# Kernel tuning notes

Measured on AMD Instinct MI355X. Metric: run time of the kernel, lower is better.

## Reference

```python
import jax, jax.numpy as jnp
import numpy as np

B, T, D = 8, 2048, 256
EPS_NORM = 1e-8
EPS_LN = 1e-6


def _layer_norm(x, gamma, beta):
    mu = jnp.mean(x, axis=-1, keepdims=True)
    var = jnp.var(x, axis=-1, keepdims=True)
    return (x - mu) * jax.lax.rsqrt(var + EPS_LN) * gamma + beta


def setup_inputs() -> dict:
    key = jax.random.key(0)
    ks = jax.random.split(key, 8)
    xav = np.sqrt(2.0 / (D + D)).astype(np.float32)  # xavier_uniform-ish scale
    a_fea = jax.random.normal(ks[0], (B, T, D), jnp.float32)
    v_fea = jax.random.normal(ks[1], (B, T, D), jnp.float32)
    Wv1 = jax.random.normal(ks[2], (D, D), jnp.float32) * xav
    Wv2 = jax.random.normal(ks[3], (D, D), jnp.float32) * xav
    Wa1 = jax.random.normal(ks[4], (D, D), jnp.float32) * xav
    Wa2 = jax.random.normal(ks[5], (D, D), jnp.float32) * xav
    ln_gamma = jnp.ones((D,), jnp.float32)
    ln_beta = jnp.zeros((D,), jnp.float32)
    thr_val = jnp.asarray(0.099, jnp.float32)
    return {"a_fea": a_fea, "v_fea": v_fea, "Wv1": Wv1, "Wv2": Wv2,
            "Wa1": Wa1, "Wa2": Wa2, "ln_gamma": ln_gamma, "ln_beta": ln_beta,
            "thr_val": thr_val}


def reference(a_fea, v_fea, Wv1, Wv2, Wa1, Wa2, ln_gamma, ln_beta, thr_val):
    # Dropout is identity in eval mode. Linear(bias=False): x @ W^T; here W is [in, out].
    v_b1 = jax.nn.relu(jnp.einsum('btd,dh->bth', v_fea, Wv1))
    v_b2 = jax.nn.relu(jnp.einsum('btd,dh->bth', v_fea, Wv2))
    a_b1 = jax.nn.relu(jnp.einsum('btd,dh->bth', a_fea, Wa1))
    a_b2 = jax.nn.relu(jnp.einsum('btd,dh->bth', a_fea, Wa2))

    scale = 1.0 / jnp.sqrt(jnp.asarray(v_b2.shape[2], jnp.float32))
    # relu-gated cross-modal scores [B, Tv, Ta]
    beta = jax.nn.relu(jnp.einsum('bvh,bah->bva', v_b2, a_b1) * scale)

    # v->a: normalize over audio axis, threshold-sparsify
    beta_va = beta / (jnp.sum(beta, axis=-1, keepdims=True) + EPS_NORM)
    gamma_va = jnp.where(beta_va > thr_val, beta_va, 0.0)
    # a->v: transpose of UN-normalized beta (faithful to source ordering)
    beta_av = jnp.swapaxes(beta, 1, 2)
    beta_av = beta_av / (jnp.sum(beta_av, axis=-1, keepdims=True) + EPS_NORM)
    gamma_av = jnp.where(beta_av > thr_val, beta_av, 0.0)

    a_pos = jnp.einsum('bva,bah->bvh', gamma_va, a_b2)
    v_pos = jnp.einsum('bav,bvh->bah', gamma_av, v_b1)

    v_psp = _layer_norm(v_fea + a_pos, ln_gamma, ln_beta)
    a_psp = _layer_norm(a_fea + v_pos, ln_gamma, ln_beta)
    return (v_psp + a_psp) * 0.5
```

## Files before the change

### kernel.cpp

```cpp
#include <hip/hip_runtime.h>
#include <stdint.h>

#define B_ 8
#define T_ 2048
#define D_ 256
#define M_ (B_*T_)

typedef uint16_t u16;
typedef __attribute__((ext_vector_type(8))) short   short8;
typedef __attribute__((ext_vector_type(8))) __bf16  bf16x8;
typedef __attribute__((ext_vector_type(4))) float   f32x4;
typedef __attribute__((ext_vector_type(4))) uint32_t u32x4;

__device__ __forceinline__ float bf2f(u16 b){
    union { uint32_t u; float f; } v; v.u = ((uint32_t)b) << 16; return v.f;
}
__device__ __forceinline__ u16 f2bf(float f){
    union { float f; uint32_t u; } v; v.f = f;
    uint32_t u = v.u;
    u += 0x7FFFu + ((u >> 16) & 1u);
    return (u16)(u >> 16);
}

typedef __attribute__((address_space(1))) void gvoid;
typedef __attribute__((address_space(3))) void lvoid;
__device__ __forceinline__ void gl16(const void* g, void* l){
    __builtin_amdgcn_global_load_lds((gvoid*)(unsigned long long)g, (lvoid*)l, 16, 0, 0);
}

__global__ void k_detect(const uint32_t* g, int* flag){
    *flag = (g[0] == 0x3F803F80u) ? 0 : 1;
}

struct WtArgs { const void* w[4]; u16* wt[4]; const int* flag; };

__global__ __launch_bounds__(256) void k_wt(WtArgs a){
    int f32in = *a.flag;
    int m = blockIdx.y;
    int d = blockIdx.x;
    int h = threadIdx.x;
    float val;
    if (f32in) val = ((const float*)a.w[m])[(size_t)d * D_ + h];
    else       val = bf2f(((const u16*)a.w[m])[(size_t)d * D_ + h]);
    a.wt[m][(size_t)h * D_ + d] = f2bf(val);
}

struct ProjArgs { const void* x[4]; const u16* wt[4]; u16* y[4]; u16* yt[4]; const int* flag; };

__global__ __launch_bounds__(256) void k_proj(ProjArgs args){
    __shared__ __align__(16) u16 Xs[128][72];
    __shared__ __align__(16) u16 Ws[128][72];
    int f32in = *args.flag;
    int id = blockIdx.x;
    int m  = id & 127;
    int vh = id >> 7;
    int hh = vh & 1;
    int v  = vh >> 1;
    const u16* Wt = args.wt[v];
    u16*       Y  = args.y[v];
    u16*       YT = args.yt[v];
    int t_base = m * 128;
    int h_base = hh * 128;

    int tid  = threadIdx.x;
    int w    = tid >> 6, lane = tid & 63;
    int wm   = w >> 1, wn = w & 1;
    int l15  = lane & 15, quad = lane >> 4;

    int srow = tid >> 1;
    int shalf = tid & 1;

    f32x4 acc[4][4];
#pragma unroll
    for (int i = 0; i < 4; ++i)
#pragma unroll
        for (int j = 0; j < 4; ++j) acc[i][j] = (f32x4){0.f,0.f,0.f,0.f};

    float4 pXf[8];
    short8 pXb[4];
    short8 pW[4];

    const float* Xf = (const float*)args.x[v] + (size_t)(t_base + srow)*D_ + shalf*32;
    const u16*   Xb = (const u16*)args.x[v]   + (size_t)(t_base + srow)*D_ + shalf*32;
    const u16*   Wp = Wt + (size_t)(h_base + srow)*D_ + shalf*32;

    if (f32in){
#pragma unroll
        for (int i = 0; i < 8; ++i) pXf[i] = *(const float4*)(Xf + i*4);
    } else {
#pragma unroll
        for (int i = 0; i < 4; ++i) pXb[i] = *(const short8*)(Xb + i*8);
    }
#pragma unroll
    for (int i = 0; i < 4; ++i) pW[i] = *(const short8*)(Wp + i*8);

    for (int k0 = 0; k0 < D_; k0 += 64){
        __syncthreads();
        if (f32in){
#pragma unroll
            for (int i = 0; i < 4; ++i){
                float4 a0 = pXf[i*2], a1 = pXf[i*2+1];
                short8 o;
                o[0]=(short)f2bf(a0.x); o[1]=(short)f2bf(a0.y); o[2]=(short)f2bf(a0.z); o[3]=(short)f2bf(a0.w);
                o[4]=(short)f2bf(a1.x); o[5]=(short)f2bf(a1.y); o[6]=(short)f2bf(a1.z); o[7]=(short)f2bf(a1.w);
                *(short8*)(&Xs[srow][shalf*32 + i*8]) = o;
            }
        } else {
#pragma unroll
            for (int i = 0; i < 4; ++i) *(short8*)(&Xs[srow][shalf*32 + i*8]) = pXb[i];
        }
#pragma unroll
        for (int i = 0; i < 4; ++i) *(short8*)(&Ws[srow][shalf*32 + i*8]) = pW[i];

        int kn = k0 + 64;
        if (kn < D_){
            if (f32in){
#pragma unroll
                for (int i = 0; i < 8; ++i) pXf[i] = *(const float4*)(Xf + kn + i*4);
            } else {
#pragma unroll
                for (int i = 0; i < 4; ++i) pXb[i] = *(const short8*)(Xb + kn + i*8);
            }
#pragma unroll
            for (int i = 0; i < 4; ++i) pW[i] = *(const short8*)(Wp + kn + i*8);
        }
        __syncthreads();

#pragma unroll
        for (int kc = 0; kc < 2; ++kc){
            bf16x8 af[4], bf[4];
#pragma unroll
            for (int i = 0; i < 4; ++i){
                af[i] = __builtin_bit_cast(bf16x8,
                         *(const short8*)(&Xs[wm*64 + i*16 + l15][kc*32 + quad*8]));
                bf[i] = __builtin_bit_cast(bf16x8,
                         *(const short8*)(&Ws[wn*64 + i*16 + l15][kc*32 + quad*8]));
            }
#pragma unroll
            for (int mt = 0; mt < 4; ++mt)
#pragma unroll
                for (int nt = 0; nt < 4; ++nt)
                    acc[mt][nt] = __builtin_amdgcn_mfma_f32_16x16x32_bf16(
                                      af[mt], bf[nt], acc[mt][nt], 0, 0, 0);
        }
    }

    int v0 = t_base + wm*64;
    int h0 = h_base + wn*64;
#pragma unroll
    for (int mt = 0; mt < 4; ++mt){
#pragma unroll
        for (int nt = 0; nt < 4; ++nt){
            int col = h0 + nt*16 + l15;
            u16 q[4];
#pragma unroll
            for (int r = 0; r < 4; ++r){
                float s = acc[mt][nt][r]; s = s > 0.f ? s : 0.f;
                q[r] = f2bf(s);
            }
            if (Y){
#pragma unroll
                for (int r = 0; r < 4; ++r)
                    Y[(size_t)(v0 + mt*16 + quad*4 + r)*D_ + col] = q[r];
            }
            if (YT){
                int row0 = v0 + mt*16 + quad*4;
                int bb   = row0 >> 11;
                int tl   = row0 & (T_-1);
                uint2 pk;
                pk.x = (uint32_t)q[0] | ((uint32_t)q[1] << 16);
                pk.y = (uint32_t)q[2] | ((uint32_t)q[3] << 16);
                *(uint2*)(YT + ((size_t)(bb*D_ + col))*T_ + tl) = pk;
            }
        }
    }
}

__global__ __launch_bounds__(256) void k_score(const u16* vb2, const u16* ab1,
                                               u16* beta, u16* betaT,
                                               float* rowsum, float* colsum){
    __shared__ __align__(16) u16 As[128][72];
    __shared__ __align__(16) u16 Bs[128][72];
    int id = blockIdx.x;
    int b  = id & 7;
    int t  = id >> 3;
    int mb = t & 15;
    int ab = t >> 4;
    int tid  = threadIdx.x;
    int w    = tid >> 6, lane = tid & 63;
    int wm   = w >> 1, wn = w & 1;
    int l15  = lane & 15, quad = lane >> 4;
    int v_base = mb*128;
    int a_base = ab*128;

    const u16* vb = vb2 + (size_t)b*T_*D_;
    const u16* an = ab1 + (size_t)b*T_*D_;
    u16*   bbp = beta  + (size_t)b*T_*T_;
    u16*   bbt = betaT + (size_t)b*T_*T_;
    float* rs  = rowsum + b*T_;
    float* cs  = colsum + b*T_;

    int kk = tid & 7;
    int mm = tid >> 3;

    f32x4 acc[4][4];
#pragma unroll
    for (int i = 0; i < 4; ++i)
#pragma unroll
        for (int j = 0; j < 4; ++j) acc[i][j] = (f32x4){0.f,0.f,0.f,0.f};

    short8 pA[4], pB[4];
#pragma unroll
    for (int i = 0; i < 4; ++i){
        int row = mm + i*32;
        pA[i] = *(const short8*)(vb + (size_t)(v_base + row)*D_ + kk*8);
        pB[i] = *(const short8*)(an + (size_t)(a_base + row)*D_ + kk*8);
    }

    for (int k0 = 0; k0 < D_; k0 += 64){
        __syncthreads();
#pragma unroll
        for (int i = 0; i < 4; ++i){
            int row = mm + i*32;
            *(short8*)(&As[row][kk*8]) = pA[i];
            *(short8*)(&Bs[row][kk*8]) = pB[i];
        }
        int kn = k0 + 64;
        if (kn < D_){
#pragma unroll
            for (int i = 0; i < 4; ++i){
                int row = mm + i*32;
                pA[i] = *(const short8*)(vb + (size_t)(v_base + row)*D_ + kn + kk*8);
                pB[i] = *(const short8*)(an + (size_t)(a_base + row)*D_ + kn + kk*8);
            }
        }
        __syncthreads();

#pragma unroll
        for (int kc = 0; kc < 2; ++kc){
            bf16x8 af[4], bf[4];
#pragma unroll
            for (int i = 0; i < 4; ++i){
                af[i] = __builtin_bit_cast(bf16x8,
                         *(const short8*)(&As[wm*64 + i*16 + l15][kc*32 + quad*8]));
                bf[i] = __builtin_bit_cast(bf16x8,
                         *(const short8*)(&Bs[wn*64 + i*16 + l15][kc*32 + quad*8]));
            }
#pragma unroll
            for (int mt = 0; mt < 4; ++mt)
#pragma unroll
                for (int nt = 0; nt < 4; ++nt)
                    acc[mt][nt] = __builtin_amdgcn_mfma_f32_16x16x32_bf16(
                                      af[mt], bf[nt], acc[mt][nt], 0, 0, 0);
        }
    }

    int v0 = v_base + wm*64;
    int a0 = a_base + wn*64;
    float rsum[4][4];
    float csum[4] = {0.f,0.f,0.f,0.f};
#pragma unroll
    for (int mt = 0; mt < 4; ++mt)
#pragma unroll
        for (int r = 0; r < 4; ++r) rsum[mt][r] = 0.f;

#pragma unroll
    for (int mt = 0; mt < 4; ++mt){
#pragma unroll
        for (int nt = 0; nt < 4; ++nt){
            u16 q[4];
#pragma unroll
            for (int r = 0; r < 4; ++r){
                float s = acc[mt][nt][r] * 0.0625f;
                s = s > 0.f ? s : 0.f;
                q[r] = f2bf(s);
                bbp[(size_t)(v0 + mt*16 + quad*4 + r)*T_ + a0 + nt*16 + l15] = q[r];
                rsum[mt][r] += s;
                csum[nt]    += s;
            }
            uint2 pk;
            pk.x = (uint32_t)q[0] | ((uint32_t)q[1] << 16);
            pk.y = (uint32_t)q[2] | ((uint32_t)q[3] << 16);
            *(uint2*)(bbt + (size_t)(a0 + nt*16 + l15)*T_ + v0 + mt*16 + quad*4) = pk;
        }
    }
#pragma unroll
    for (int mt = 0; mt < 4; ++mt){
#pragma unroll
        for (int r = 0; r < 4; ++r){
            float v = rsum[mt][r];
            v += __shfl_xor(v, 1);
            v += __shfl_xor(v, 2);
            v += __shfl_xor(v, 4);
            v += __shfl_xor(v, 8);
            if (l15 == 0) atomicAdd(&rs[v0 + mt*16 + quad*4 + r], v);
        }
    }
#pragma unroll
    for (int nt = 0; nt < 4; ++nt){
        float v = csum[nt];
        v += __shfl_xor(v, 16);
        v += __shfl_xor(v, 32);
        if (quad == 0) atomicAdd(&cs[a0 + nt*16 + l15], v);
    }
}

__global__ __launch_bounds__(256) void k_pos4(const u16* beta, const u16* betaT,
                                              const u16* ab2T, const u16* vb1T,
                                              const float* rowsum, const float* colsum,
                                              const void* thrp, const int* flag,
                                              u16* apos, u16* vpos){
    __shared__ __align__(16) u16 SL[2][2][128*64];
    int f32in = *flag;
    int id = blockIdx.x;
    int nb    = id & 1;
    int mb    = (id >> 1) & 15;
    int b     = (id >> 5) & 7;
    int which = id >> 8;

    const u16* A   = (which ? betaT : beta) + (size_t)b*T_*T_;
    const u16* Bt  = (which ? vb1T  : ab2T) + (size_t)b*T_*D_;
    const float* nrm = (which ? colsum : rowsum) + b*T_;
    u16* outb = (which ? vpos : apos) + (size_t)b*T_*D_;

    float thr = f32in ? *(const float*)thrp : bf2f(*(const u16*)thrp);

    int tid = threadIdx.x;
    int w = tid >> 6, lane = tid & 63;
    int l15 = lane & 15, quad = lane >> 4;

    int m0 = mb * 128;
    int h0 = nb * 128;

    int srow = w*32 + (lane >> 3);
    int schk = (lane & 7) ^ ((lane >> 3) & 7);
    const u16* gA = A  + (size_t)(m0 + srow)*T_ + schk*8;
    const u16* gB = Bt + (size_t)(h0 + srow)*T_ + schk*8;

    uint32_t thp[2];
#pragma unroll
    for (int i = 0; i < 2; ++i){
        float ts = thr * (nrm[m0 + w*32 + i*16 + l15] + 1e-8f);
        union { float f; uint32_t u; } cv; cv.f = ts;
        uint32_t th16 = cv.u >> 16;
        thp[i] = th16 * 0x10001u;
    }

    f32x4 acc[2][8];
#pragma unroll
    for (int i = 0; i < 2; ++i)
#pragma unroll
        for (int j = 0; j < 8; ++j) acc[i][j] = (f32x4){0.f,0.f,0.f,0.f};

#pragma unroll
    for (int c = 0; c < 4; ++c){
        gl16(gA + (size_t)c*8*T_, &SL[0][0][(w*32 + c*8)*64]);
        gl16(gB + (size_t)c*8*T_, &SL[0][1][(w*32 + c*8)*64]);
    }

    int q = 0;
    for (int k0 = 0; k0 < T_; k0 += 64){
        __syncthreads();
        int kn = k0 + 64;
        if (kn < T_){
#pragma unroll
            for (int c = 0; c < 4; ++c){
                gl16(gA + (size_t)c*8*T_ + kn, &SL[q^1][0][(w*32 + c*8)*64]);
                gl16(gB + (size_t)c*8*T_ + kn, &SL[q^1][1][(w*32 + c*8)*64]);
            }
        }
        const u16* Asb = &SL[q][0][0];
        const u16* Bsb = &SL[q][1][0];
#pragma unroll
        for (int kc = 0; kc < 2; ++kc){
            int sw = ((kc*4 + quad) ^ (l15 & 7)) * 8;
            bf16x8 af[2];
#pragma unroll
            for (int i = 0; i < 2; ++i){
                u32x4 ra = *(const u32x4*)(Asb + (size_t)(w*32 + i*16 + l15)*64 + sw);
                u32x4 om;
#pragma unroll
                for (int jd = 0; jd < 4; ++jd){
                    uint32_t t, m;
                    asm("v_pk_sub_u16 %0, %1, %2" : "=v"(t) : "v"(thp[i]), "v"(ra[jd]));
                    asm("v_pk_ashrrev_i16 %0, 15, %1" : "=v"(m) : "v"(t));
                    om[jd] = ra[jd] & m;
                }
                af[i] = __builtin_bit_cast(bf16x8, om);
            }
#pragma unroll
            for (int nt = 0; nt < 8; ++nt){
                bf16x8 bfr = __builtin_bit_cast(bf16x8,
                              *(const short8*)(Bsb + (size_t)(nt*16 + l15)*64 + sw));
                acc[0][nt] = __builtin_amdgcn_mfma_f32_16x16x32_bf16(
                                  af[0], bfr, acc[0][nt], 0, 0, 0);
                acc[1][nt] = __builtin_amdgcn_mfma_f32_16x16x32_bf16(
                                  af[1], bfr, acc[1][nt], 0, 0, 0);
            }
        }
        q ^= 1;
    }

#pragma unroll
    for (int i = 0; i < 2; ++i){
#pragma unroll
        for (int r = 0; r < 4; ++r){
            int row = m0 + w*32 + i*16 + quad*4 + r;
            float iv = 1.f / (nrm[row] + 1e-8f);
#pragma unroll
            for (int nt = 0; nt < 8; ++nt)
                outb[(size_t)row*D_ + h0 + nt*16 + l15] =
                    f2bf(acc[i][nt][r] * iv);
        }
    }
}

__global__ __launch_bounds__(256) void k_ln(const void* vfea, const void* afea,
                                            const u16* apos, const u16* vpos,
                                            const void* g, const void* lnb,
                                            const int* flag, void* out){
    int f32in = *flag;
    int row = blockIdx.x;
    int c   = threadIdx.x;
    size_t idx = (size_t)row * D_ + c;
    float xv = f32in ? ((const float*)vfea)[idx] : bf2f(((const u16*)vfea)[idx]);
    float xa = f32in ? ((const float*)afea)[idx] : bf2f(((const u16*)afea)[idx]);
    float x1 = xv + bf2f(apos[idx]);
    float x2 = xa + bf2f(vpos[idx]);
    float s1 = x1, q1 = x1*x1, s2 = x2, q2 = x2*x2;
#pragma unroll
    for (int off = 1; off < 64; off <<= 1){
        s1 += __shfl_xor(s1, off);
        q1 += __shfl_xor(q1, off);
        s2 += __shfl_xor(s2, off);
        q2 += __shfl_xor(q2, off);
    }
    __shared__ float red[4][4];
    int wave = threadIdx.x >> 6;
    if ((threadIdx.x & 63) == 0){
        red[0][wave] = s1; red[1][wave] = q1; red[2][wave] = s2; red[3][wave] = q2;
    }
    __syncthreads();
    s1 = red[0][0]+red[0][1]+red[0][2]+red[0][3];
    q1 = red[1][0]+red[1][1]+red[1][2]+red[1][3];
    s2 = red[2][0]+red[2][1]+red[2][2]+red[2][3];
    q2 = red[3][0]+red[3][1]+red[3][2]+red[3][3];
    const float invD = 1.f / (float)D_;
    float mu1 = s1*invD, mu2 = s2*invD;
    float var1 = q1*invD - mu1*mu1;
    float var2 = q2*invD - mu2*mu2;
    float rs1 = rsqrtf(var1 + 1e-6f);
    float rs2 = rsqrtf(var2 + 1e-6f);
    float gg = f32in ? ((const float*)g)[c]   : bf2f(((const u16*)g)[c]);
    float bv = f32in ? ((const float*)lnb)[c] : bf2f(((const u16*)lnb)[c]);
    float y = 0.5f * (((x1-mu1)*rs1)*gg + bv + ((x2-mu2)*rs2)*gg + bv);
    if (f32in) ((float*)out)[idx] = y;
    else       ((u16*)out)[idx]   = f2bf(y);
}

extern "C" void kernel_launch(void* const* d_in, const int* in_sizes, int n_in,
                              void* d_out, int out_size, void* d_ws, size_t ws_size,
                              hipStream_t stream){
    (void)in_sizes; (void)n_in; (void)out_size; (void)ws_size;
    const void* a_fea = d_in[0];
    const void* v_fea = d_in[1];
    const void* Wv1   = d_in[2];
    const void* Wv2   = d_in[3];
    const void* Wa1   = d_in[4];
    const void* Wa2   = d_in[5];
    const void* lng   = d_in[6];
    const void* lnb   = d_in[7];
    const void* thrp  = d_in[8];
    char* ws = (char*)d_ws;

    const size_t ACT  = (size_t)M_ * D_ * 2;
    const size_t BETA = (size_t)B_ * T_ * T_ * 2;
    size_t off_wt    = 0;
    size_t off_vb2   = 524288;
    size_t off_ab1   = off_vb2  + ACT;
    size_t off_vb1T  = off_ab1  + ACT;
    size_t off_ab2T  = off_vb1T + ACT;
    size_t off_beta  = off_ab2T + ACT;
    size_t off_betaT = off_beta  + BETA;
    size_t off_rsum  = off_betaT + BETA;
    size_t off_csum  = off_rsum + (size_t)B_*T_*4;
    size_t off_apos  = off_csum + (size_t)B_*T_*4;
    size_t off_vpos  = off_apos + ACT;
    size_t off_flag  = off_vpos + ACT;

    u16* wt0   = (u16*)(ws + off_wt);
    u16* vb2   = (u16*)(ws + off_vb2);
    u16* ab1   = (u16*)(ws + off_ab1);
    u16* vb1T  = (u16*)(ws + off_vb1T);
    u16* ab2T  = (u16*)(ws + off_ab2T);
    u16* beta  = (u16*)(ws + off_beta);
    u16* betaT = (u16*)(ws + off_betaT);
    float* rowsum = (float*)(ws + off_rsum);
    float* colsum = (float*)(ws + off_csum);
    u16*   apos   = (u16*)(ws + off_apos);
    u16*   vpos   = (u16*)(ws + off_vpos);
    int*   flag   = (int*)(ws + off_flag);

    hipMemsetAsync(ws + off_rsum, 0, 2 * (size_t)B_ * T_ * sizeof(float), stream);

    k_detect<<<1, 1, 0, stream>>>((const uint32_t*)lng, flag);

    WtArgs wa;
    wa.w[0] = Wv1; wa.w[1] = Wv2; wa.w[2] = Wa1; wa.w[3] = Wa2;
    for (int i = 0; i < 4; ++i) wa.wt[i] = wt0 + (size_t)i * D_ * D_;
    wa.flag = flag;
    k_wt<<<dim3(256,4), 256, 0, stream>>>(wa);

    ProjArgs pa;
    pa.x[0] = v_fea; pa.x[1] = v_fea; pa.x[2] = a_fea; pa.x[3] = a_fea;
    for (int i = 0; i < 4; ++i) pa.wt[i] = wa.wt[i];
    pa.y[0] = nullptr; pa.y[1] = vb2; pa.y[2] = ab1; pa.y[3] = nullptr;
    pa.yt[0] = vb1T;   pa.yt[1] = nullptr; pa.yt[2] = nullptr; pa.yt[3] = ab2T;
    pa.flag = flag;
    k_proj<<<4*2*(M_/128), 256, 0, stream>>>(pa);

    k_score<<<8*16*16, 256, 0, stream>>>(vb2, ab1, beta, betaT, rowsum, colsum);

    k_pos4<<<512, 256, 0, stream>>>(beta, betaT, ab2T, vb1T, rowsum, colsum,
                                    thrp, flag, apos, vpos);

    k_ln<<<M_, 256, 0, stream>>>(v_fea, a_fea, apos, vpos, lng, lnb, flag, d_out);
}
```

Baseline: 247.9 us.

## Store beta once in tiled layout and read its transpose via ds_read_b64_tr_b16

The score kernel no longer writes a separate transposed copy of the beta matrix. It writes beta once, in 128x128 tiles. The aggregation kernel loads those tiles directly for the v->a side and uses the LDS transpose-read instruction to get transposed fragments for the a->v side. This removes one 64MB write and the scattered transposed stores, at the cost of a more complex LDS load path with an explicit waitcnt. Block indices are also remapped so that blocks from the same batch are interleaved across XCDs.

```diff
diff --git a/kernel.cpp b/kernel.cpp
--- a/kernel.cpp
+++ b/kernel.cpp
@@ -24,6 +24,7 @@
 
 typedef __attribute__((address_space(1))) void gvoid;
 typedef __attribute__((address_space(3))) void lvoid;
+typedef __attribute__((address_space(3))) const u16 lds_cu16;
 __device__ __forceinline__ void gl16(const void* g, void* l){
     __builtin_amdgcn_global_load_lds((gvoid*)(unsigned long long)g, (lvoid*)l, 16, 0, 0);
 }
@@ -177,7 +178,7 @@
 }
 
 __global__ __launch_bounds__(256) void k_score(const u16* vb2, const u16* ab1,
-                                               u16* beta, u16* betaT,
+                                               u16* beta_t,
                                                float* rowsum, float* colsum){
     __shared__ __align__(16) u16 As[128][72];
     __shared__ __align__(16) u16 Bs[128][72];
@@ -195,8 +196,7 @@
 
     const u16* vb = vb2 + (size_t)b*T_*D_;
     const u16* an = ab1 + (size_t)b*T_*D_;
-    u16*   bbp = beta  + (size_t)b*T_*T_;
-    u16*   bbt = betaT + (size_t)b*T_*T_;
+    u16* tb = beta_t + (((size_t)b*16 + mb)*16 + ab)*16384;
     float* rs  = rowsum + b*T_;
     float* cs  = colsum + b*T_;
 
@@ -255,8 +255,6 @@
         }
     }
 
-    int v0 = v_base + wm*64;
-    int a0 = a_base + wn*64;
     float rsum[4][4];
     float csum[4] = {0.f,0.f,0.f,0.f};
 #pragma unroll
@@ -268,22 +266,19 @@
     for (int mt = 0; mt < 4; ++mt){
 #pragma unroll
         for (int nt = 0; nt < 4; ++nt){
-            u16 q[4];
+            int aa = wn*64 + nt*16 + l15;
 #pragma unroll
             for (int r = 0; r < 4; ++r){
                 float s = acc[mt][nt][r] * 0.0625f;
                 s = s > 0.f ? s : 0.f;
-                q[r] = f2bf(s);
-                bbp[(size_t)(v0 + mt*16 + quad*4 + r)*T_ + a0 + nt*16 + l15] = q[r];
+                tb[(size_t)(wm*64 + mt*16 + quad*4 + r)*128 + aa] = f2bf(s);
                 rsum[mt][r] += s;
                 csum[nt]    += s;
             }
-            uint2 pk;
-            pk.x = (uint32_t)q[0] | ((uint32_t)q[1] << 16);
-            pk.y = (uint32_t)q[2] | ((uint32_t)q[3] << 16);
-            *(uint2*)(bbt + (size_t)(a0 + nt*16 + l15)*T_ + v0 + mt*16 + quad*4) = pk;
-        }
-    }
+        }
+    }
+    int v0 = v_base + wm*64;
+    int a0 = a_base + wn*64;
 #pragma unroll
     for (int mt = 0; mt < 4; ++mt){
 #pragma unroll
@@ -305,20 +300,21 @@
     }
 }
 
-__global__ __launch_bounds__(256) void k_pos4(const u16* beta, const u16* betaT,
+__global__ __launch_bounds__(256) void k_pos6(const u16* beta_t,
                                               const u16* ab2T, const u16* vb1T,
                                               const float* rowsum, const float* colsum,
                                               const void* thrp, const int* flag,
                                               u16* apos, u16* vpos){
     __shared__ __align__(16) u16 SL[2][2][128*64];
     int f32in = *flag;
-    int id = blockIdx.x;
+    int s  = blockIdx.x;
+    int id = (s & 7) * 64 + (s >> 3);
     int nb    = id & 1;
     int mb    = (id >> 1) & 15;
     int b     = (id >> 5) & 7;
     int which = id >> 8;
 
-    const u16* A   = (which ? betaT : beta) + (size_t)b*T_*T_;
+    const u16* TB  = beta_t + (size_t)b*16*16*16384;
     const u16* Bt  = (which ? vb1T  : ab2T) + (size_t)b*T_*D_;
     const float* nrm = (which ? colsum : rowsum) + b*T_;
     u16* outb = (which ? vpos : apos) + (size_t)b*T_*D_;
@@ -332,10 +328,11 @@
     int m0 = mb * 128;
     int h0 = nb * 128;
 
-    int srow = w*32 + (lane >> 3);
     int schk = (lane & 7) ^ ((lane >> 3) & 7);
-    const u16* gA = A  + (size_t)(m0 + srow)*T_ + schk*8;
-    const u16* gB = Bt + (size_t)(h0 + srow)*T_ + schk*8;
+    const u16* gB = Bt + (size_t)(h0 + w*32 + (lane >> 3))*T_ + schk*8;
+
+    int vl = ((lane >> 3) & 3)*8 + ((lane >> 5) & 1)*4 + ((lane >> 1) & 3);
+    int ha = lane & 1;
 
     uint32_t thp[2];
 #pragma unroll
@@ -352,22 +349,52 @@
 #pragma unroll
         for (int j = 0; j < 8; ++j) acc[i][j] = (f32x4){0.f,0.f,0.f,0.f};
 
-#pragma unroll
-    for (int c = 0; c < 4; ++c){
-        gl16(gA + (size_t)c*8*T_, &SL[0][0][(w*32 + c*8)*64]);
+    if (which == 0){
+#pragma unroll
+        for (int c = 0; c < 4; ++c){
+            const u16* src = TB + ((size_t)mb*16 + 0)*16384
+                           + (size_t)(w*32 + c*8 + (lane>>3))*128 + schk*8;
+            gl16(src, &SL[0][0][(w*32 + c*8)*64]);
+        }
+    } else {
+#pragma unroll
+        for (int p = 0; p < 4; ++p){
+            int sa = w*2 + (p & 1), kc = p >> 1;
+            const u16* src = TB + ((size_t)0*16 + mb)*16384
+                           + (size_t)(kc*32 + vl)*128 + sa*16 + ha*8;
+            gl16(src, (u16*)SL[0][0] + sa*1024 + kc*512);
+        }
+    }
+#pragma unroll
+    for (int c = 0; c < 4; ++c)
         gl16(gB + (size_t)c*8*T_, &SL[0][1][(w*32 + c*8)*64]);
-    }
 
     int q = 0;
     for (int k0 = 0; k0 < T_; k0 += 64){
         __syncthreads();
         int kn = k0 + 64;
         if (kn < T_){
-#pragma unroll
-            for (int c = 0; c < 4; ++c){
-                gl16(gA + (size_t)c*8*T_ + kn, &SL[q^1][0][(w*32 + c*8)*64]);
+            if (which == 0){
+                int at = kn >> 7, col0 = kn & 127;
+#pragma unroll
+                for (int c = 0; c < 4; ++c){
+                    const u16* src = TB + ((size_t)mb*16 + at)*16384
+                                   + (size_t)(w*32 + c*8 + (lane>>3))*128 + col0 + schk*8;
+                    gl16(src, &SL[q^1][0][(w*32 + c*8)*64]);
+                }
+            } else {
+                int vt = kn >> 7, v0 = kn & 127;
+#pragma unroll
+                for (int p = 0; p < 4; ++p){
+                    int sa = w*2 + (p & 1), kc = p >> 1;
+                    const u16* src = TB + ((size_t)vt*16 + mb)*16384
+                                   + (size_t)(v0 + kc*32 + vl)*128 + sa*16 + ha*8;
+                    gl16(src, (u16*)SL[q^1][0] + sa*1024 + kc*512);
+                }
+            }
+#pragma unroll
+            for (int c = 0; c < 4; ++c)
                 gl16(gB + (size_t)c*8*T_ + kn, &SL[q^1][1][(w*32 + c*8)*64]);
-            }
         }
         const u16* Asb = &SL[q][0][0];
         const u16* Bsb = &SL[q][1][0];
@@ -375,18 +402,45 @@
         for (int kc = 0; kc < 2; ++kc){
             int sw = ((kc*4 + quad) ^ (l15 & 7)) * 8;
             bf16x8 af[2];
-#pragma unroll
-            for (int i = 0; i < 2; ++i){
-                u32x4 ra = *(const u32x4*)(Asb + (size_t)(w*32 + i*16 + l15)*64 + sw);
-                u32x4 om;
-#pragma unroll
-                for (int jd = 0; jd < 4; ++jd){
-                    uint32_t t, m;
-                    asm("v_pk_sub_u16 %0, %1, %2" : "=v"(t) : "v"(thp[i]), "v"(ra[jd]));
-                    asm("v_pk_ashrrev_i16 %0, 15, %1" : "=v"(m) : "v"(t));
-                    om[jd] = ra[jd] & m;
+            if (which == 0){
+#pragma unroll
+                for (int i = 0; i < 2; ++i){
+                    u32x4 ra = *(const u32x4*)(Asb + (size_t)(w*32 + i*16 + l15)*64 + sw);
+                    u32x4 om;
+#pragma unroll
+                    for (int jd = 0; jd < 4; ++jd){
+                        uint32_t tt, mm2;
+                        asm("v_pk_sub_u16 %0, %1, %2" : "=v"(tt) : "v"(thp[i]), "v"(ra[jd]));
+                        asm("v_pk_ashrrev_i16 %0, 15, %1" : "=v"(mm2) : "v"(tt));
+                        om[jd] = ra[jd] & mm2;
+                    }
+                    af[i] = __builtin_bit_cast(bf16x8, om);
                 }
-                af[i] = __builtin_bit_cast(bf16x8, om);
+            } else {
+                uint2 t0[2], t1[2];
+#pragma unroll
+                for (int i = 0; i < 2; ++i){
+                    lds_cu16* pa = (lds_cu16*)(Asb + (w*2 + i)*1024 + kc*512 + lane*4);
+                    asm volatile("ds_read_b64_tr_b16 %0, %1"
+                                 : "=v"(t0[i]) : "v"(pa) : "memory");
+                    asm volatile("ds_read_b64_tr_b16 %0, %1 offset:512"
+                                 : "=v"(t1[i]) : "v"(pa) : "memory");
+                }
+                asm volatile("s_waitcnt lgkmcnt(0)" ::: "memory");
+                __builtin_amdgcn_sched_barrier(0);
+#pragma unroll
+                for (int i = 0; i < 2; ++i){
+                    u32x4 ra = {t0[i].x, t0[i].y, t1[i].x, t1[i].y};
+                    u32x4 om;
+#pragma unroll
+                    for (int jd = 0; jd < 4; ++jd){
+                        uint32_t tt, mm2;
+                        asm("v_pk_sub_u16 %0, %1, %2" : "=v"(tt) : "v"(thp[i]), "v"(ra[jd]));
+                        asm("v_pk_ashrrev_i16 %0, 15, %1" : "=v"(mm2) : "v"(tt));
+                        om[jd] = ra[jd] & mm2;
+                    }
+                    af[i] = __builtin_bit_cast(bf16x8, om);
+                }
             }
 #pragma unroll
             for (int nt = 0; nt < 8; ++nt){
@@ -481,8 +535,7 @@
     size_t off_vb1T  = off_ab1  + ACT;
     size_t off_ab2T  = off_vb1T + ACT;
     size_t off_beta  = off_ab2T + ACT;
-    size_t off_betaT = off_beta  + BETA;
-    size_t off_rsum  = off_betaT + BETA;
+    size_t off_rsum  = off_beta + BETA;
     size_t off_csum  = off_rsum + (size_t)B_*T_*4;
     size_t off_apos  = off_csum + (size_t)B_*T_*4;
     size_t off_vpos  = off_apos + ACT;
@@ -494,7 +547,6 @@
     u16* vb1T  = (u16*)(ws + off_vb1T);
     u16* ab2T  = (u16*)(ws + off_ab2T);
     u16* beta  = (u16*)(ws + off_beta);
-    u16* betaT = (u16*)(ws + off_betaT);
     float* rowsum = (float*)(ws + off_rsum);
     float* colsum = (float*)(ws + off_csum);
     u16*   apos   = (u16*)(ws + off_apos);
@@ -519,9 +571,9 @@
     pa.flag = flag;
     k_proj<<<4*2*(M_/128), 256, 0, stream>>>(pa);
 
-    k_score<<<8*16*16, 256, 0, stream>>>(vb2, ab1, beta, betaT, rowsum, colsum);
-
-    k_pos4<<<512, 256, 0, stream>>>(beta, betaT, ab2T, vb1T, rowsum, colsum,
+    k_score<<<8*16*16, 256, 0, stream>>>(vb2, ab1, beta, rowsum, colsum);
+
+    k_pos6<<<512, 256, 0, stream>>>(beta, ab2T, vb1T, rowsum, colsum,
                                     thrp, flag, apos, vpos);
 
     k_ln<<<M_, 256, 0, stream>>>(v_fea, a_fea, apos, vpos, lng, lnb, flag, d_out);
```

Result: faster. 222.9 us (-10.1%).
